# Optimization experiments

Hardware: AMD Instinct MI355X
Metric: run time of the kernel (lower is better)

The kernel has to match this reference:

```python
import jax, jax.numpy as jnp
import numpy as np

B, T, D_MODEL = 2, 2048, 2048
H, HD = 16, 128          # num_heads, head_dim
KV_L, Q_L, R = 512, 1024, 64  # kv_latent, q_latent, qk_rope_dim


def apply_rope(x, freqs):
    # x: (..., T, R); freqs: (T, R//2) angles theta (torch stores exp(i*theta))
    # torch pairs consecutive elements: view(..., R//2, 2) as complex
    xr = x.reshape(x.shape[:-1] + (R // 2, 2))
    x0, x1 = xr[..., 0], xr[..., 1]
    cos, sin = jnp.cos(freqs), jnp.sin(freqs)  # broadcast over leading dims
    y0 = x0 * cos - x1 * sin
    y1 = x0 * sin + x1 * cos
    return jnp.stack([y0, y1], axis=-1).reshape(x.shape)


def setup_inputs() -> dict:
    key = jax.random.key(0)
    ks = jax.random.split(key, 10)
    s = 0.02
    return {
        "x": jax.random.normal(ks[0], (B, T, D_MODEL), jnp.float32),
        "freqs": jax.random.normal(ks[1], (T, R // 2), jnp.float32),
        # weights stored as (in, out) so forward is x @ W (== torch x @ W.T)
        "W_DKV": jax.random.normal(ks[2], (D_MODEL, KV_L), jnp.float32) * s,
        "W_UK": jax.random.normal(ks[3], (KV_L, H * HD), jnp.float32) * s,
        "W_UV": jax.random.normal(ks[4], (KV_L, H * HD), jnp.float32) * s,
        "W_KR": jax.random.normal(ks[5], (D_MODEL, R), jnp.float32) * s,
        "W_DQ": jax.random.normal(ks[6], (D_MODEL, Q_L), jnp.float32) * s,
        "W_UQ": jax.random.normal(ks[7], (Q_L, H * HD), jnp.float32) * s,
        "W_QR": jax.random.normal(ks[8], (Q_L, H * R), jnp.float32) * s,
        "W_O": jax.random.normal(ks[9], (H * HD, D_MODEL), jnp.float32) * s,
    }


def reference(x, freqs, W_DKV, W_UK, W_UV, W_KR, W_DQ, W_UQ, W_QR, W_O):
    b, t, _ = x.shape
    # compressed KV latent and expansions
    c_KV = x @ W_DKV                                             # (B,T,KV_L)
    K_c = (c_KV @ W_UK).reshape(b, t, H, HD).transpose(0, 2, 1, 3)  # (B,H,T,HD)
    V = (c_KV @ W_UV).reshape(b, t, H, HD).transpose(0, 2, 1, 3)    # (B,H,T,HD)
    # shared (single-head) rope key
    K_r1 = apply_rope((x @ W_KR)[:, None, :, :], freqs)          # (B,1,T,R)
    K_r = jnp.broadcast_to(K_r1, (b, H, t, R))
    # compressed Q latent
    c_Q = x @ W_DQ                                               # (B,T,Q_L)
    Q_c = (c_Q @ W_UQ).reshape(b, t, H, HD).transpose(0, 2, 1, 3)
    Q_r = apply_rope((c_Q @ W_QR).reshape(b, t, H, R).transpose(0, 2, 1, 3), freqs)
    Q = jnp.concatenate([Q_c, Q_r], axis=-1)                     # (B,H,T,HD+R)
    K = jnp.concatenate([K_c, K_r], axis=-1)
    # causal SDPA, scale = 1/sqrt(HD+R) (torch default: query last dim)
    scale = 1.0 / jnp.sqrt(jnp.asarray(HD + R, Q.dtype))
    scores = jnp.einsum("bhqe,bhke->bhqk", Q, K) * scale
    causal = jnp.tril(jnp.ones((t, t), bool))
    scores = jnp.where(causal, scores, jnp.asarray(-1e30, scores.dtype))
    attn = jax.nn.softmax(scores, axis=-1)
    out = jnp.einsum("bhqk,bhkd->bhqd", attn, V)                 # (B,H,T,HD)
    out = out.transpose(0, 2, 1, 3).reshape(b, t, H * HD)
    y = out @ W_O                                                # (B,T,D_MODEL)
    return (y, c_KV, K_r1[:, 0, :, :])
```

## Files before the change

### kernel.cpp

```cpp
#include <hip/hip_runtime.h>
#include <stdint.h>

typedef unsigned short u16;
typedef __attribute__((ext_vector_type(8))) short s16x8;
typedef __attribute__((ext_vector_type(4))) float f32x4;

#define B_   2
#define T_   2048
#define DM   2048
#define H_   16
#define HD_  128
#define R_   64
#define E_   192
#define SCALE2 0.104117542f

__device__ __forceinline__ u16 f2b(float f) {
  union { float f; uint32_t u; } x; x.f = f;
  uint32_t u = x.u;
  return (u16)((u + 0x7FFFu + ((u >> 16) & 1u)) >> 16);
}
__device__ __forceinline__ float b2f(u16 h) {
  union { uint32_t u; float f; } x; x.u = ((uint32_t)h) << 16;
  return x.f;
}
__device__ __forceinline__ unsigned pk2(float a, float b) {
  union { float f; unsigned u; } A, B; A.f = a; B.f = b;
  return (B.u & 0xFFFF0000u) | (A.u >> 16);
}
__device__ __forceinline__ void ld_lds16(const void* g, void* l) {
  __builtin_amdgcn_global_load_lds((const __attribute__((address_space(1))) void*)g,
                                   (__attribute__((address_space(3))) void*)l,
                                   16, 0, 0);
}

__device__ __forceinline__ void conv_dev(const float* __restrict__ in, u16* __restrict__ out, int i) {
  float4 v = *(const float4*)(in + (size_t)i * 4);
  ushort4 o;
  o.x = f2b(v.x); o.y = f2b(v.y); o.z = f2b(v.z); o.w = f2b(v.w);
  *(ushort4*)(out + (size_t)i * 4) = o;
}
__device__ __forceinline__ void tr64(const float* __restrict__ in, u16* __restrict__ out,
                                     int K, int N, int bx, int by) {
  __shared__ u16 t[64][65];
  int bn = bx * 64, bk = by * 64;
  int tid = threadIdx.x;
  int r0 = tid >> 4, c0 = (tid & 15) * 4;
#pragma unroll
  for (int rr = 0; rr < 64; rr += 16) {
    float4 v = *(const float4*)(in + (size_t)(bk + r0 + rr) * N + bn + c0);
    t[r0 + rr][c0 + 0] = f2b(v.x); t[r0 + rr][c0 + 1] = f2b(v.y);
    t[r0 + rr][c0 + 2] = f2b(v.z); t[r0 + rr][c0 + 3] = f2b(v.w);
  }
  __syncthreads();
#pragma unroll
  for (int rr = 0; rr < 64; rr += 16) {
    ushort4 v;
    v.x = t[c0 + 0][r0 + rr]; v.y = t[c0 + 1][r0 + rr];
    v.z = t[c0 + 2][r0 + rr]; v.w = t[c0 + 3][r0 + rr];
    *(ushort4*)(out + (size_t)(bn + r0 + rr) * K + bk + c0) = v;
  }
}

__global__ __launch_bounds__(256)
void ta_k(const float* __restrict__ x, const float* __restrict__ fr,
          u16* __restrict__ x_bf, u16* __restrict__ fr_bf,
          const float* __restrict__ wdkv, const float* __restrict__ wkr,
          const float* __restrict__ wdq, u16* __restrict__ W,
          const float* __restrict__ wuk, const float* __restrict__ wuv,
          const float* __restrict__ wuq, const float* __restrict__ wqr,
          u16* __restrict__ UKUV, u16* __restrict__ UQQR) {
  int id = blockIdx.x;
  if (id < 8192)        conv_dev(x, x_bf, id * 256 + threadIdx.x);
  else if (id < 8256)   conv_dev(fr, fr_bf, (id - 8192) * 256 + threadIdx.x);
  else if (id < 8512) { int i = id - 8256; tr64(wdkv, W, 2048, 512, i & 7, i >> 3); }
  else if (id < 8544) { int i = id - 8512; tr64(wkr, W + 512 * 2048, 2048, 64, 0, i); }
  else if (id < 9056) { int i = id - 8544; tr64(wdq, W + 576 * 2048, 2048, 1024, i & 15, i >> 4); }
  else if (id < 9312) { int i = id - 9056; tr64(wuk, UKUV, 512, 2048, i & 31, i >> 5); }
  else if (id < 9568) { int i = id - 9312; tr64(wuv, UKUV + 2048 * 512, 512, 2048, i & 31, i >> 5); }
  else if (id < 10080){ int i = id - 9568; tr64(wuq, UQQR, 1024, 2048, i & 31, i >> 5); }
  else                { int i = id - 10080; tr64(wqr, UQQR + 2048 * 1024, 1024, 1024, i & 15, i >> 4); }
}
__global__ __launch_bounds__(256)
void tb1_k(const float* __restrict__ wuk, const float* __restrict__ wuv, u16* __restrict__ W) {
  int id = blockIdx.x;
  if (id < 256) tr64(wuk, W, 512, 2048, id & 31, id >> 5);
  else { int i = id - 256; tr64(wuv, W + 2048 * 512, 512, 2048, i & 31, i >> 5); }
}
__global__ __launch_bounds__(256)
void tb2_k(const float* __restrict__ wuq, const float* __restrict__ wqr, u16* __restrict__ W) {
  int id = blockIdx.x;
  if (id < 512) tr64(wuq, W, 1024, 2048, id & 31, id >> 5);
  else { int i = id - 512; tr64(wqr, W + 2048 * 1024, 1024, 1024, i & 15, i >> 4); }
}
__global__ __launch_bounds__(256)
void tc_k(const float* __restrict__ wo, u16* __restrict__ W) {
  tr64(wo, W, 2048, 2048, blockIdx.x & 31, blockIdx.x >> 5);
}

template <int EPI>
__device__ __forceinline__ void gemm_body(u16* Al, u16* Bl,
               const u16* __restrict__ A, const u16* __restrict__ Bt,
               u16* __restrict__ O0, u16* __restrict__ O1, u16* __restrict__ O2,
               float* __restrict__ OF, float* __restrict__ OF2,
               const u16* __restrict__ FR, int M, int N, int K, int bx, int by) {
  const int tid = threadIdx.x;
  const int ln = tid & 63, w = tid >> 6;
  const int quad = ln >> 4, l16 = ln & 15;
  const int wm = (w >> 1) * 64, wn = (w & 1) * 64;
  const int m0 = by * 128, n0 = bx * 128;

  f32x4 zz = {0.f, 0.f, 0.f, 0.f};
  f32x4 acc[4][4];
#pragma unroll
  for (int i = 0; i < 4; i++)
#pragma unroll
    for (int j = 0; j < 4; j++) acc[i][j] = zz;

  const u16* aG[2];
  const u16* bG[2];
  int ldsC[2];
#pragma unroll
  for (int r = 0; r < 2; r++) {
    int i = tid + r * 256;
    int row = i >> 2, cq = (i & 3) * 8;
    aG[r] = A + (size_t)(m0 + row) * K + cq;
    int rb = n0 + row;
    if (rb > N - 1) rb = N - 1;
    bG[r] = Bt + (size_t)rb * K + cq;
    ldsC[r] = ((tid & ~63) + r * 256) * 8;
  }

  for (int k = 0; k < K; k += 64) {
#pragma unroll
    for (int hh = 0; hh < 2; hh++)
#pragma unroll
      for (int r = 0; r < 2; r++) {
        ld_lds16(aG[r] + k + hh * 32, &Al[hh * 4096 + ldsC[r]]);
        ld_lds16(bG[r] + k + hh * 32, &Bl[hh * 4096 + ldsC[r]]);
      }
    __syncthreads();
#pragma unroll
    for (int hh = 0; hh < 2; hh++) {
      s16x8 af[4], bf[4];
#pragma unroll
      for (int f = 0; f < 4; f++)
        af[f] = *(const s16x8*)&Al[hh * 4096 + (wm + f * 16 + l16) * 32 + quad * 8];
#pragma unroll
      for (int f = 0; f < 4; f++)
        bf[f] = *(const s16x8*)&Bl[hh * 4096 + (wn + f * 16 + l16) * 32 + quad * 8];
#pragma unroll
      for (int i = 0; i < 4; i++)
#pragma unroll
        for (int j = 0; j < 4; j++)
          acc[i][j] = __builtin_amdgcn_mfma_f32_16x16x32_bf16(af[i], bf[j], acc[i][j], 0, 0, 0);
    }
    __syncthreads();
  }

#pragma unroll
  for (int fm = 0; fm < 4; fm++) {
#pragma unroll
    for (int fn = 0; fn < 4; fn++) {
      int n = n0 + wn + fn * 16 + l16;
      int mb = m0 + wm + fm * 16 + quad * 4;
      if (EPI == 2) {
        if (n < N) {
#pragma unroll
          for (int rg = 0; rg < 4; rg++) OF[(size_t)(mb + rg) * N + n] = acc[fm][fn][rg];
        }
      } else if (EPI == 4) {
        if (n < 2048) {
#pragma unroll
          for (int rg = 0; rg < 4; rg++) O0[(size_t)(mb + rg) * 2048 + n] = f2b(acc[fm][fn][rg]);
        } else {
          int hd = n - 2048, b = mb >> 11, t = mb & 2047;
          ushort4 v;
          v.x = f2b(acc[fm][fn][0]); v.y = f2b(acc[fm][fn][1]);
          v.z = f2b(acc[fm][fn][2]); v.w = f2b(acc[fm][fn][3]);
          *(ushort4*)(O1 + ((size_t)(b * 2048 + hd) * 2048 + t)) = v;
        }
      } else if (EPI == 5) {
        if (n < 2048) {
#pragma unroll
          for (int rg = 0; rg < 4; rg++) O0[(size_t)(mb + rg) * 2048 + n] = f2b(acc[fm][fn][rg]);
        } else {
#pragma unroll
          for (int rg = 0; rg < 4; rg++) O1[(size_t)(mb + rg) * 1024 + (n - 2048)] = f2b(acc[fm][fn][rg]);
        }
      } else {
        if (n < 512) {
#pragma unroll
          for (int rg = 0; rg < 4; rg++) {
            float v = acc[fm][fn][rg];
            O0[(size_t)(mb + rg) * 512 + n] = f2b(v);
            OF[(size_t)(mb + rg) * 512 + n] = v;
          }
        } else if (n < 576) {
          int r = n - 512, r2 = r >> 1, odd = r & 1;
#pragma unroll
          for (int rg = 0; rg < 4; rg++) {
            float v = acc[fm][fn][rg];
            float p = __shfl_xor(v, 1);
            int t = mb + rg;
            float a = b2f(FR[(size_t)(t & 2047) * 32 + r2]);
            float sn, cs;
            __sincosf(a, &sn, &cs);
            float y = odd ? (p * sn + v * cs) : (v * cs - p * sn);
            O1[(size_t)t * 64 + r] = f2b(y);
            OF2[(size_t)t * 64 + r] = y;
          }
        } else if (n < 1600) {
#pragma unroll
          for (int rg = 0; rg < 4; rg++) O2[(size_t)(mb + rg) * 1024 + (n - 576)] = f2b(acc[fm][fn][rg]);
        }
      }
    }
  }
}

template <int EPI>
__global__ __launch_bounds__(256)
void gemm_bf16(const u16* __restrict__ A, const u16* __restrict__ Bt,
               u16* __restrict__ O0, u16* __restrict__ O1, u16* __restrict__ O2,
               float* __restrict__ OF, float* __restrict__ OF2,
               const u16* __restrict__ FR, int M, int N, int K) {
  __shared__ __align__(16) u16 Al[2 * 128 * 32];
  __shared__ __align__(16) u16 Bl[2 * 128 * 32];
  gemm_body<EPI>(Al, Bl, A, Bt, O0, O1, O2, OF, OF2, FR, M, N, K, blockIdx.x, blockIdx.y);
}

__global__ __launch_bounds__(256)
void kvq_k(const u16* __restrict__ cKV, const u16* __restrict__ UKUV,
           u16* __restrict__ Kc, u16* __restrict__ VT,
           const u16* __restrict__ cQ, const u16* __restrict__ UQQR,
           u16* __restrict__ Qc, u16* __restrict__ Qr,
           const float* __restrict__ wo, u16* __restrict__ W) {
  __shared__ __align__(16) u16 Al[2 * 128 * 32];
  __shared__ __align__(16) u16 Bl[2 * 128 * 32];
  int id = blockIdx.x;
  if (id < 768) {
    gemm_body<5>(Al, Bl, cQ, UQQR, Qc, Qr, nullptr, nullptr, nullptr, nullptr,
                 4096, 3072, 1024, id % 24, id / 24);
  } else if (id < 1792) {
    int j = id - 768;
    gemm_body<4>(Al, Bl, cKV, UKUV, Kc, VT, nullptr, nullptr, nullptr, nullptr,
                 4096, 4096, 512, j & 31, j >> 5);
  } else {
    int j = id - 1792;
    tr64(wo, W, 2048, 2048, j & 31, j >> 5);
  }
}

#define KT_S 200
#define VT_S 72
__global__ __launch_bounds__(512, 2)
void flash_attn(const u16* __restrict__ Qc, const u16* __restrict__ Qr,
                const u16* __restrict__ Kc, const u16* __restrict__ Kr,
                const u16* __restrict__ VT, const u16* __restrict__ fr,
                u16* __restrict__ O) {
  __shared__ __align__(16) u16 Kt[64 * KT_S];
  __shared__ __align__(16) u16 Vt[144 * VT_S];

  const int tid = threadIdx.x;
  const int ln = tid & 63, w = tid >> 6;
  const int quad = ln >> 4, l16 = ln & 15;
  const int bh = blockIdx.x, b = bh >> 4, h = bh & 15;

  for (int i = tid; i < 1024; i += 512) Vt[(128 + (i >> 6)) * VT_S + (i & 63)] = 0x3F80;

  const u16* kBase[3]; int kStep[3], kLds[3];
#pragma unroll
  for (int r = 0; r < 3; r++) {
    int i = tid + r * 512;
    int key = i / 24, c = i - key * 24;
    kLds[r] = key * KT_S + c * 8;
    if (c < 16) { kBase[r] = Kc + ((size_t)(b * T_ + key) * DM + h * HD_ + c * 8); kStep[r] = 64 * DM; }
    else        { kBase[r] = Kr + ((size_t)(b * T_ + key) * R_ + (c - 16) * 8);    kStep[r] = 64 * R_; }
  }
  const u16* vBase[2]; int vLds[2];
#pragma unroll
  for (int r = 0; r < 2; r++) {
    int i = tid + r * 512;
    int row = i >> 3, c = i & 7, c2 = c & 3;
    vLds[r] = row * VT_S + (c >> 2) * 32 + ((2 * c2) & 3) * 8 + (c2 >> 1) * 4;
    vBase[r] = VT + ((size_t)(bh * HD_ + row) * T_ + c * 8);
  }

  f32x4 zz = {0.f, 0.f, 0.f, 0.f};
  const int q0 = (15 - (int)blockIdx.y) * 128;
  const int qw = q0 + w * 16;

  s16x8 qf[6];
  {
    int t = qw + l16;
    const u16* p = Qc + ((size_t)(b * T_ + t) * DM + h * HD_ + quad * 8);
#pragma unroll
    for (int f = 0; f < 4; f++) qf[f] = *(const s16x8*)(p + f * 32);
    const u16* pr = Qr + ((size_t)(b * T_ + t) * (H_ * R_) + h * R_ + quad * 8);
#pragma unroll
    for (int half = 0; half < 2; half++) {
      s16x8 v = *(const s16x8*)(pr + half * 32);
      s16x8 o2;
#pragma unroll
      for (int p2 = 0; p2 < 4; p2++) {
        float a = b2f(fr[t * 32 + half * 16 + quad * 4 + p2]);
        float sn, cs;
        __sincosf(a, &sn, &cs);
        float x0 = b2f((u16)v[2 * p2]), x1 = b2f((u16)v[2 * p2 + 1]);
        o2[2 * p2] = (short)f2b(x0 * cs - x1 * sn);
        o2[2 * p2 + 1] = (short)f2b(x0 * sn + x1 * cs);
      }
      qf[4 + half] = o2;
    }
  }

  f32x4 o[9];
#pragma unroll
  for (int f = 0; f < 9; f++) o[f] = zz;
  float mL = -1e30f;

  const u16* pk[3]; const u16* pv[2];
  s16x8 kv[3], vv[2];
#pragma unroll
  for (int r = 0; r < 3; r++) { pk[r] = kBase[r]; kv[r] = *(const s16x8*)pk[r]; }
#pragma unroll
  for (int r = 0; r < 2; r++) { pv[r] = vBase[r]; vv[r] = *(const s16x8*)pv[r]; }

  const int nk = q0 + 128;
  for (int k0 = 0; k0 < nk; k0 += 64) {
    __syncthreads();
#pragma unroll
    for (int r = 0; r < 3; r++) *(s16x8*)&Kt[kLds[r]] = kv[r];
#pragma unroll
    for (int r = 0; r < 2; r++) {
      union { s16x8 v; uint4 u; } V_; V_.v = vv[r];
      uint2 lo; lo.x = V_.u.x; lo.y = V_.u.y;
      uint2 hi; hi.x = V_.u.z; hi.y = V_.u.w;
      *(uint2*)&Vt[vLds[r]] = lo;
      *(uint2*)&Vt[vLds[r] + 8] = hi;
    }
    __syncthreads();
    if (k0 + 64 < nk) {
#pragma unroll
      for (int r = 0; r < 3; r++) { pk[r] += kStep[r]; kv[r] = *(const s16x8*)pk[r]; }
#pragma unroll
      for (int r = 0; r < 2; r++) { pv[r] += 64; vv[r] = *(const s16x8*)pv[r]; }
    }
    if (k0 > qw + 15) continue;

    f32x4 s[4];
#pragma unroll
    for (int kg = 0; kg < 4; kg++) s[kg] = zz;
#pragma unroll
    for (int e = 0; e < 6; e++)
#pragma unroll
      for (int kg = 0; kg < 4; kg++) {
        s16x8 kf = *(const s16x8*)&Kt[(kg * 16 + l16) * KT_S + e * 32 + quad * 8];
        s[kg] = __builtin_amdgcn_mfma_f32_16x16x32_bf16(kf, qf[e], s[kg], 0, 0, 0);
      }
    const int q = qw + l16;
    float sv[16];
    if (k0 + 63 <= qw) {
#pragma unroll
      for (int kg = 0; kg < 4; kg++)
#pragma unroll
        for (int rg = 0; rg < 4; rg++) sv[kg * 4 + rg] = s[kg][rg] * SCALE2;
    } else {
#pragma unroll
      for (int kg = 0; kg < 4; kg++)
#pragma unroll
        for (int rg = 0; rg < 4; rg++) {
          int key = k0 + kg * 16 + quad * 4 + rg;
          sv[kg * 4 + rg] = (key > q) ? -1e30f : s[kg][rg] * SCALE2;
        }
    }
    float mxa = fmaxf(fmaxf(sv[0], sv[1]), fmaxf(sv[2], sv[3]));
    float mxb = fmaxf(fmaxf(sv[4], sv[5]), fmaxf(sv[6], sv[7]));
    float mxc = fmaxf(fmaxf(sv[8], sv[9]), fmaxf(sv[10], sv[11]));
    float mxd = fmaxf(fmaxf(sv[12], sv[13]), fmaxf(sv[14], sv[15]));
    float mx = fmaxf(fmaxf(mxa, mxb), fmaxf(mxc, mxd));
    mx = fmaxf(mx, __shfl_xor(mx, 16));
    mx = fmaxf(mx, __shfl_xor(mx, 32));
    if (__any(mx > mL)) {
      float mn = fmaxf(mL, mx);
      float alpha = exp2f(mL - mn);
      mL = mn;
      float al[4];
#pragma unroll
      for (int rg = 0; rg < 4; rg++) al[rg] = __shfl(alpha, (ln & 48) | (quad * 4 + rg));
#pragma unroll
      for (int f = 0; f < 9; f++)
#pragma unroll
        for (int rg = 0; rg < 4; rg++) o[f][rg] *= al[rg];
    }
    float p[16];
#pragma unroll
    for (int j = 0; j < 16; j++) p[j] = exp2f(sv[j] - mL);
    union { unsigned pw[8]; s16x8 pa[2]; } P_;
#pragma unroll
    for (int kg = 0; kg < 4; kg++) {
      P_.pw[kg * 2 + 0] = pk2(p[kg * 4 + 0], p[kg * 4 + 1]);
      P_.pw[kg * 2 + 1] = pk2(p[kg * 4 + 2], p[kg * 4 + 3]);
    }
#pragma unroll
    for (int f = 0; f < 9; f++) {
      s16x8 vb0 = *(const s16x8*)&Vt[(f * 16 + l16) * VT_S + quad * 8];
      o[f] = __builtin_amdgcn_mfma_f32_16x16x32_bf16(P_.pa[0], vb0, o[f], 0, 0, 0);
      s16x8 vb1 = *(const s16x8*)&Vt[(f * 16 + l16) * VT_S + 32 + quad * 8];
      o[f] = __builtin_amdgcn_mfma_f32_16x16x32_bf16(P_.pa[1], vb1, o[f], 0, 0, 0);
    }
  }

  float inv[4];
#pragma unroll
  for (int rg = 0; rg < 4; rg++) inv[rg] = 1.0f / o[8][rg];
#pragma unroll
  for (int f = 0; f < 8; f++) {
#pragma unroll
    for (int rg = 0; rg < 4; rg++) {
      int qq = qw + quad * 4 + rg;
      O[(size_t)(b * T_ + qq) * DM + h * HD_ + f * 16 + l16] = f2b(o[f][rg] * inv[rg]);
    }
  }
}

extern "C" void kernel_launch(void* const* d_in, const int* in_sizes, int n_in,
                              void* d_out, int out_size, void* d_ws, size_t ws_size,
                              hipStream_t stream) {
  const float* x    = (const float*)d_in[0];
  const float* fr   = (const float*)d_in[1];
  const float* wdkv = (const float*)d_in[2];
  const float* wuk  = (const float*)d_in[3];
  const float* wuv  = (const float*)d_in[4];
  const float* wkr  = (const float*)d_in[5];
  const float* wdq  = (const float*)d_in[6];
  const float* wuq  = (const float*)d_in[7];
  const float* wqr  = (const float*)d_in[8];
  const float* wo   = (const float*)d_in[9];
  u16* ws = (u16*)d_ws;

  const size_t M1 = 1048576;
  u16* x_bf  = ws;
  u16* Om    = ws;
  u16* Kc    = ws + 8 * M1;
  u16* VTm   = ws + 16 * M1;
  u16* Qc    = ws + 24 * M1;
  u16* Qr    = ws + 32 * M1;
  u16* W     = ws + 36 * M1;
  u16* cKV   = ws + 40 * M1;
  u16* cQ    = ws + 42 * M1;
  u16* fr_bf = ws + 46 * M1;
  u16* kr_bf = fr_bf + 65536;
  u16* UKUV  = ws + 47 * M1;
  u16* UQQR  = ws + 49 * M1;

  float* out_y   = (float*)d_out;
  float* out_ckv = (float*)d_out + 8388608;
  float* out_kr  = (float*)d_out + 10485760;
  (void)in_sizes; (void)n_in; (void)out_size;

  dim3 blk(256);
  const bool merged = ws_size >= (size_t)52 * M1 * 2;

  if (merged) {
    ta_k<<<dim3(10336), blk, 0, stream>>>(x, fr, x_bf, fr_bf, wdkv, wkr, wdq, W,
                                          wuk, wuv, wuq, wqr, UKUV, UQQR);
    gemm_bf16<6><<<dim3(13, 32), blk, 0, stream>>>(x_bf, W, cKV, kr_bf, cQ, out_ckv, out_kr, fr_bf,
                                                   4096, 1600, 2048);
    kvq_k<<<dim3(2816), blk, 0, stream>>>(cKV, UKUV, Kc, VTm, cQ, UQQR, Qc, Qr, wo, W);
  } else {
    ta_k<<<dim3(9056), blk, 0, stream>>>(x, fr, x_bf, fr_bf, wdkv, wkr, wdq, W,
                                         wuk, wuv, wuq, wqr, UKUV, UQQR);
    gemm_bf16<6><<<dim3(13, 32), blk, 0, stream>>>(x_bf, W, cKV, kr_bf, cQ, out_ckv, out_kr, fr_bf,
                                                   4096, 1600, 2048);
    tb1_k<<<dim3(512), blk, 0, stream>>>(wuk, wuv, W);
    gemm_bf16<4><<<dim3(32, 32), blk, 0, stream>>>(cKV, W, Kc, VTm, nullptr, nullptr, nullptr,
                                                   nullptr, 4096, 4096, 512);
    tb2_k<<<dim3(768), blk, 0, stream>>>(wuq, wqr, W);
    gemm_bf16<5><<<dim3(24, 32), blk, 0, stream>>>(cQ, W, Qc, Qr, nullptr, nullptr, nullptr,
                                                   nullptr, 4096, 3072, 1024);
  }
  flash_attn<<<dim3(32, 16), dim3(512), 0, stream>>>(Qc, Qr, Kc, kr_bf, VTm, fr_bf, Om);
  if (!merged) {
    tc_k<<<dim3(1024), blk, 0, stream>>>(wo, W);
  }
  gemm_bf16<2><<<dim3(16, 32), blk, 0, stream>>>(Om, W, nullptr, nullptr, nullptr, out_y, nullptr,
                                                 nullptr, 4096, 2048, 2048);
}
```

Measured before the change: 374.1 us.

## Stage transposed V-cache stores through LDS and defer softmax max rescaling

Adds a new GEMM epilogue for the V half of the K/V up-projection. It writes bf16 results into a per-wave LDS tile and then emits coalesced 16-byte stores into the transposed V buffer, replacing scattered 8-byte transposed writes. The kvq kernel's shared memory is enlarged into one buffer to hold this staging area. Separately, flash attention now rescales its running max only when the new max exceeds the old by more than 8 in log2 units, skipping most rescales. That lazy rescale risks larger unnormalised exponentials, bounded by 2^8 in fp32, and the wider LDS allocation may reduce occupancy.

```diff
diff --git a/kernel.cpp b/kernel.cpp
--- a/kernel.cpp
+++ b/kernel.cpp
@@ -26,6 +26,9 @@
 __device__ __forceinline__ unsigned pk2(float a, float b) {
   union { float f; unsigned u; } A, B; A.f = a; B.f = b;
   return (B.u & 0xFFFF0000u) | (A.u >> 16);
+}
+__device__ __forceinline__ unsigned pku(u16 a, u16 b) {
+  return (unsigned)a | ((unsigned)b << 16);
 }
 __device__ __forceinline__ void ld_lds16(const void* g, void* l) {
   __builtin_amdgcn_global_load_lds((const __attribute__((address_space(1))) void*)g,
@@ -187,6 +190,16 @@
 #pragma unroll
           for (int rg = 0; rg < 4; rg++) O1[(size_t)(mb + rg) * 1024 + (n - 2048)] = f2b(acc[fm][fn][rg]);
         }
+      } else if (EPI == 7) {
+        if (n0 < 2048) {
+#pragma unroll
+          for (int rg = 0; rg < 4; rg++) O0[(size_t)(mb + rg) * 2048 + n] = f2b(acc[fm][fn][rg]);
+        } else {
+          u16* Lw = Al + w * 4224;
+          int cl = fn * 16 + l16, rb = fm * 16 + quad * 4;
+          *(unsigned*)&Lw[cl * 66 + rb]     = pku(f2b(acc[fm][fn][0]), f2b(acc[fm][fn][1]));
+          *(unsigned*)&Lw[cl * 66 + rb + 2] = pku(f2b(acc[fm][fn][2]), f2b(acc[fm][fn][3]));
+        }
       } else {
         if (n < 512) {
 #pragma unroll
@@ -216,6 +229,25 @@
       }
     }
   }
+  if (EPI == 7) {
+    if (n0 >= 2048) {
+      __asm__ volatile("s_waitcnt lgkmcnt(0)" ::: "memory");
+      u16* Lw = Al + w * 4224;
+      int hd0 = n0 - 2048 + wn;
+      int t0g = m0 + wm;
+      int bb = t0g >> 11, tl = t0g & 2047;
+#pragma unroll
+      for (int i = 0; i < 8; i++) {
+        int cl = (ln >> 3) + i * 8;
+        int toff = (ln & 7) * 8;
+        const u16* ls = &Lw[cl * 66 + toff];
+        uint4 v;
+        v.x = *(const unsigned*)(ls + 0); v.y = *(const unsigned*)(ls + 2);
+        v.z = *(const unsigned*)(ls + 4); v.w = *(const unsigned*)(ls + 6);
+        *(uint4*)&O1[((size_t)(bb * 2048 + hd0 + cl) * 2048) + tl + toff] = v;
+      }
+    }
+  }
 }
 
 template <int EPI>
@@ -235,15 +267,14 @@
            const u16* __restrict__ cQ, const u16* __restrict__ UQQR,
            u16* __restrict__ Qc, u16* __restrict__ Qr,
            const float* __restrict__ wo, u16* __restrict__ W) {
-  __shared__ __align__(16) u16 Al[2 * 128 * 32];
-  __shared__ __align__(16) u16 Bl[2 * 128 * 32];
+  __shared__ __align__(16) u16 SH[16896];
   int id = blockIdx.x;
   if (id < 768) {
-    gemm_body<5>(Al, Bl, cQ, UQQR, Qc, Qr, nullptr, nullptr, nullptr, nullptr,
+    gemm_body<5>(SH, SH + 8192, cQ, UQQR, Qc, Qr, nullptr, nullptr, nullptr, nullptr,
                  4096, 3072, 1024, id % 24, id / 24);
   } else if (id < 1792) {
     int j = id - 768;
-    gemm_body<4>(Al, Bl, cKV, UKUV, Kc, VT, nullptr, nullptr, nullptr, nullptr,
+    gemm_body<7>(SH, SH + 8192, cKV, UKUV, Kc, VT, nullptr, nullptr, nullptr, nullptr,
                  4096, 4096, 512, j & 31, j >> 5);
   } else {
     int j = id - 1792;
@@ -381,7 +412,7 @@
     float mx = fmaxf(fmaxf(mxa, mxb), fmaxf(mxc, mxd));
     mx = fmaxf(mx, __shfl_xor(mx, 16));
     mx = fmaxf(mx, __shfl_xor(mx, 32));
-    if (__any(mx > mL)) {
+    if (__any(mx > mL + 8.0f)) {
       float mn = fmaxf(mL, mx);
       float alpha = exp2f(mL - mn);
       mL = mn;
```

Result: no change. 367.0 us (-1.9%).
